# Kernel optimization log

Hardware: AMD Instinct MI355X
Metric: run time of the kernel (lower is better)

Reference implementation:

```python
import jax, jax.numpy as jnp
import numpy as np

BANDWITH = 10.0  # matches init kwarg `bandwith`


def setup_inputs() -> dict:
    key = jax.random.key(0)
    kx, ky = jax.random.split(key)
    X = jax.random.normal(kx, (8192, 128), dtype=jnp.float32)
    Y = jax.random.normal(ky, (8192, 128), dtype=jnp.float32)
    return {"X": X, "Y": Y}


def reference(X, Y):
    # Z = vstack([X, Y]) : [N+M, d]
    Z = jnp.concatenate([X, Y], axis=0)
    # squared euclidean cdist: ||zi||^2 + ||zj||^2 - 2 zi.zj  (clamped >= 0)
    sq = jnp.sum(Z * Z, axis=-1)  # [N+M]
    d2 = sq[:, None] + sq[None, :] - 2.0 * jnp.matmul(Z, Z.T)
    d2 = jnp.maximum(d2, 0.0)
    # RBF kernel; the original's [None,...].sum(dim=0) over a single bandwidth is identity
    K = jnp.exp(-d2 / (2.0 * BANDWITH ** 2))  # [N+M, N+M]
    n = X.shape[0]
    XX = jnp.mean(K[:n, :n])
    XY = jnp.mean(K[:n, n:])
    YY = jnp.mean(K[n:, n:])
    return XX - 2.0 * XY + YY
```

## Files before the change

kernel.cpp:

```cpp
#include <hip/hip_runtime.h>
#include <math.h>

#define TD 128
#define BT 64
#define TB 256
#define GRID 256

typedef _Float16 half8 __attribute__((ext_vector_type(8)));
typedef _Float16 half2v __attribute__((ext_vector_type(2)));
typedef float f32x4 __attribute__((ext_vector_type(4)));

#define C2f   (-0.0072134752044448f)
#define M2C2f (0.0144269504088896f)

#if __has_builtin(__builtin_amdgcn_exp2f)
#define EXP2F(x) __builtin_amdgcn_exp2f(x)
#else
#define EXP2F(x) exp2f(x)
#endif

#define LA0 0
#define LA1 32768
#define LB0 65536
#define LB1 98304
#define LEA 131072
#define LEB 132096
#define LRED 133120
#define LDS_TOT 133152

#define FENCE() asm volatile("" ::: "memory")
#define SCHEDB() __builtin_amdgcn_sched_barrier(0)

__device__ __forceinline__ void gload16(const void* g, void* l) {
    __builtin_amdgcn_global_load_lds(
        (const __attribute__((address_space(1))) void*)g,
        (__attribute__((address_space(3))) void*)l, 16, 0, 0);
}

__device__ __forceinline__ void decode_tile(int t, int T, int& bi, int& bj) {
    double bguess = (2.0 * T + 1.0 -
                     sqrt((2.0 * T + 1.0) * (2.0 * T + 1.0) - 8.0 * (double)t)) * 0.5;
    int b = (int)bguess;
    if (b < 0) b = 0;
    if (b > T - 1) b = T - 1;
    while ((b + 1) * T - ((b + 1) * b) / 2 <= t) ++b;
    while (b * T - (b * (b - 1)) / 2 > t) --b;
    bi = b;
    bj = b + (t - (b * T - (b * (b - 1)) / 2));
}

__global__ __launch_bounds__(256) void cvt_norms_kernel(const float* __restrict__ X,
                                                        const float* __restrict__ Y,
                                                        int n, int tot,
                                                        _Float16* __restrict__ Z16,
                                                        float* __restrict__ En) {
    const int wid  = (blockIdx.x * 256 + threadIdx.x) >> 6;
    const int lane = threadIdx.x & 63;
    if (wid >= tot) return;
    const float* row = (wid < n) ? (X + (size_t)wid * TD) : (Y + (size_t)(wid - n) * TD);
    float2 v = *reinterpret_cast<const float2*>(row + lane * 2);
    _Float16 hx = (_Float16)v.x;
    _Float16 hy = (_Float16)v.y;
    half2v h2 = {hx, hy};
    *reinterpret_cast<half2v*>(Z16 + (size_t)wid * TD + lane * 2) = h2;
    float fx = (float)hx, fy = (float)hy;
    float s = fmaf(fx, fx, fy * fy);
#pragma unroll
    for (int off = 32; off > 0; off >>= 1) s += __shfl_down(s, off, 64);
    if (lane == 0) En[wid] = EXP2F(C2f * s);
}

__global__ __launch_bounds__(512, 2) void mmd_pipe_kernel(const _Float16* __restrict__ Z16,
                                                          const float* __restrict__ En,
                                                          double* __restrict__ partials,
                                                          int n, int m, int T, int ntiles) {
    __shared__ char lds[LDS_TOT];

    const int tid = threadIdx.x;
    const int l = tid & 63;
    const int w = tid >> 6;
    const int wrow = (w >> 2) * 128;
    const int wcol = (w & 3) * 64;
    const int lr = l & 15;
    const int kq = l >> 4;
    const int swz = lr & 7;

    const int rsub = l >> 3;
    const int psl  = l & 7;
    const int srcsw = (psl ^ rsub) << 4;

    int it = blockIdx.x;
    if (it >= ntiles) return;

    int bi, bj;
    decode_tile(it, T, bi, bj);

    {
        const char* gA = (const char*)(Z16 + (size_t)bi * TB * TD);
        const char* gB = (const char*)(Z16 + (size_t)bj * TB * TD);
#pragma unroll
        for (int q = 0; q < 4; ++q) {
            const int chunk = w * 4 + q;
            const int row = chunk * 8 + rsub;
            gload16(gA + (size_t)row * 256 + srcsw, lds + LA0 + chunk * 1024);
            gload16(gB + (size_t)row * 256 + srcsw, lds + LB0 + chunk * 1024);
        }
    }

    while (true) {
        {
            const char* gA = (const char*)(Z16 + (size_t)bi * TB * TD);
            const char* gB = (const char*)(Z16 + (size_t)bj * TB * TD);
#pragma unroll
            for (int q = 0; q < 4; ++q) {
                const int chunk = w * 4 + q;
                const int row = chunk * 8 + rsub;
                gload16(gA + (size_t)row * 256 + 128 + srcsw, lds + LA1 + chunk * 1024);
                gload16(gB + (size_t)row * 256 + 128 + srcsw, lds + LB1 + chunk * 1024);
            }
            if (w == 0) gload16(En + (size_t)bi * TB + l * 4, lds + LEA);
            if (w == 1) gload16(En + (size_t)bj * TB + l * 4, lds + LEB);
        }
        if (w < 2) asm volatile("s_waitcnt vmcnt(9)" ::: "memory");
        else       asm volatile("s_waitcnt vmcnt(8)" ::: "memory");
        SCHEDB();
        __builtin_amdgcn_s_barrier();
        SCHEDB();

        f32x4 acc[8][4];
        const f32x4 zero4 = {0.f, 0.f, 0.f, 0.f};
        __builtin_amdgcn_s_setprio(1);
#pragma unroll
        for (int kk = 0; kk < 2; ++kk) {
            const int soff = ((kk * 4 + kq) ^ swz) << 4;
            half8 bf[4];
#pragma unroll
            for (int j = 0; j < 4; ++j)
                bf[j] = *reinterpret_cast<const half8*>(lds + LB0 + (wcol + j * 16 + lr) * 128 + soff);
#pragma unroll
            for (int i = 0; i < 8; ++i) {
                half8 af = *reinterpret_cast<const half8*>(lds + LA0 + (wrow + i * 16 + lr) * 128 + soff);
#pragma unroll
                for (int j = 0; j < 4; ++j)
                    acc[i][j] = __builtin_amdgcn_mfma_f32_16x16x32_f16(
                        af, bf[j], (kk == 0) ? zero4 : acc[i][j], 0, 0, 0);
            }
        }
        __builtin_amdgcn_s_setprio(0);

        FENCE();
        __builtin_amdgcn_s_barrier();
        SCHEDB();

        const int itn = it + GRID;
        const bool more = (itn < ntiles);
        int bin = bi, bjn = bj;
        if (more) {
            decode_tile(itn, T, bin, bjn);
            const char* gA = (const char*)(Z16 + (size_t)bin * TB * TD);
            const char* gB = (const char*)(Z16 + (size_t)bjn * TB * TD);
#pragma unroll
            for (int q = 0; q < 4; ++q) {
                const int chunk = w * 4 + q;
                const int row = chunk * 8 + rsub;
                gload16(gA + (size_t)row * 256 + srcsw, lds + LA0 + chunk * 1024);
                gload16(gB + (size_t)row * 256 + srcsw, lds + LB0 + chunk * 1024);
            }
        }
        if (more) asm volatile("s_waitcnt vmcnt(8)" ::: "memory");
        else      asm volatile("s_waitcnt vmcnt(0)" ::: "memory");
        SCHEDB();
        __builtin_amdgcn_s_barrier();
        SCHEDB();

        __builtin_amdgcn_s_setprio(1);
#pragma unroll
        for (int kk = 0; kk < 2; ++kk) {
            const int soff = ((kk * 4 + kq) ^ swz) << 4;
            half8 bf[4];
#pragma unroll
            for (int j = 0; j < 4; ++j)
                bf[j] = *reinterpret_cast<const half8*>(lds + LB1 + (wcol + j * 16 + lr) * 128 + soff);
#pragma unroll
            for (int i = 0; i < 8; ++i) {
                half8 af = *reinterpret_cast<const half8*>(lds + LA1 + (wrow + i * 16 + lr) * 128 + soff);
#pragma unroll
                for (int j = 0; j < 4; ++j)
                    acc[i][j] = __builtin_amdgcn_mfma_f32_16x16x32_f16(af, bf[j], acc[i][j], 0, 0, 0);
            }
        }
        __builtin_amdgcn_s_setprio(0);

        float Ej[4];
#pragma unroll
        for (int j = 0; j < 4; ++j)
            Ej[j] = *reinterpret_cast<const float*>(lds + LEB + (wcol + j * 16 + lr) * 4);
        f32x4 EiV[8];
#pragma unroll
        for (int i = 0; i < 8; ++i)
            EiV[i] = *reinterpret_cast<const f32x4*>(lds + LEA + (wrow + i * 16 + kq * 4) * 4);

        float s = 0.f;
#pragma unroll
        for (int j = 0; j < 4; ++j) {
            float sj0 = 0.f, sj1 = 0.f;
#pragma unroll
            for (int i = 0; i < 8; ++i) {
#pragma unroll
                for (int r = 0; r < 4; ++r) {
                    float e = EXP2F(M2C2f * acc[i][j][r]);
                    if (r & 1) sj1 = fmaf(EiV[i][r], e, sj1);
                    else       sj0 = fmaf(EiV[i][r], e, sj0);
                }
            }
            s = fmaf(Ej[j], sj0 + sj1, s);
        }

#pragma unroll
        for (int off = 32; off > 0; off >>= 1) s += __shfl_down(s, off, 64);
        if (l == 0) *reinterpret_cast<float*>(lds + LRED + w * 4) = s;
        asm volatile("s_waitcnt lgkmcnt(0)" ::: "memory");
        SCHEDB();
        __builtin_amdgcn_s_barrier();
        SCHEDB();
        if (tid == 0) {
            const float* sred = reinterpret_cast<const float*>(lds + LRED);
            float bs = 0.f;
#pragma unroll
            for (int q = 0; q < 8; ++q) bs += sred[q];
            double wa = (bi * TB < n) ? (1.0 / (double)n) : (-1.0 / (double)m);
            double wb = (bj * TB < n) ? (1.0 / (double)n) : (-1.0 / (double)m);
            double wgt = wa * wb * ((bi == bj) ? 1.0 : 2.0);
            partials[it] = wgt * (double)bs;
        }

        if (!more) break;
        it = itn; bi = bin; bj = bjn;
    }
}

__global__ __launch_bounds__(256) void norms_kernel(const float* __restrict__ X,
                                                    const float* __restrict__ Y,
                                                    int n, int tot,
                                                    float* __restrict__ norms) {
    int r = blockIdx.x * 256 + threadIdx.x;
    if (r >= tot) return;
    const float* row = (r < n) ? (X + (size_t)r * TD) : (Y + (size_t)(r - n) * TD);
    float s = 0.f;
#pragma unroll
    for (int k = 0; k < TD; k += 4) {
        float4 v = *reinterpret_cast<const float4*>(row + k);
        s = fmaf(v.x, v.x, s); s = fmaf(v.y, v.y, s);
        s = fmaf(v.z, v.z, s); s = fmaf(v.w, v.w, s);
    }
    norms[r] = s;
}

__global__ __launch_bounds__(256, 2) void mmd_tile_kernel(const float* __restrict__ X,
                                                          const float* __restrict__ Y,
                                                          const float* __restrict__ norms,
                                                          double* __restrict__ partials,
                                                          int n, int m, int T) {
    __shared__ float sA[TD][BT];
    __shared__ float sB[TD][BT];
    __shared__ float sredf[4];

    const int t = blockIdx.x;
    int bi, bj;
    decode_tile(t, T, bi, bj);

    const int tid = threadIdx.x;
    {
        const int row = tid & 63;
        const int qb  = tid >> 6;
        const int ra = bi * BT + row;
        const int rb = bj * BT + row;
        const float* Arow = (ra < n) ? (X + (size_t)ra * TD) : (Y + (size_t)(ra - n) * TD);
        const float* Brow = (rb < n) ? (X + (size_t)rb * TD) : (Y + (size_t)(rb - n) * TD);
#pragma unroll
        for (int i = 0; i < 8; ++i) {
            const int q = qb + 4 * i;
            float4 va = *reinterpret_cast<const float4*>(Arow + 4 * q);
            sA[4 * q + 0][row] = va.x; sA[4 * q + 1][row] = va.y;
            sA[4 * q + 2][row] = va.z; sA[4 * q + 3][row] = va.w;
            float4 vb = *reinterpret_cast<const float4*>(Brow + 4 * q);
            sB[4 * q + 0][row] = vb.x; sB[4 * q + 1][row] = vb.y;
            sB[4 * q + 2][row] = vb.z; sB[4 * q + 3][row] = vb.w;
        }
    }
    __syncthreads();

    const int tx = tid & 15;
    const int ty = tid >> 4;
    float acc[4][4];
#pragma unroll
    for (int i = 0; i < 4; ++i)
#pragma unroll
        for (int j = 0; j < 4; ++j) acc[i][j] = 0.f;

#pragma unroll 16
    for (int k = 0; k < TD; ++k) {
        float4 a = *reinterpret_cast<const float4*>(&sA[k][ty * 4]);
        float4 b = *reinterpret_cast<const float4*>(&sB[k][tx * 4]);
        const float av[4] = {a.x, a.y, a.z, a.w};
        const float bv[4] = {b.x, b.y, b.z, b.w};
#pragma unroll
        for (int i = 0; i < 4; ++i)
#pragma unroll
            for (int j = 0; j < 4; ++j)
                acc[i][j] = fmaf(av[i], bv[j], acc[i][j]);
    }

    float nA[4], nB[4];
#pragma unroll
    for (int i = 0; i < 4; ++i) nA[i] = norms[bi * BT + ty * 4 + i];
#pragma unroll
    for (int j = 0; j < 4; ++j) nB[j] = norms[bj * BT + tx * 4 + j];

    const float cexp = -0.005f;
    float s = 0.f;
#pragma unroll
    for (int i = 0; i < 4; ++i)
#pragma unroll
        for (int j = 0; j < 4; ++j) {
            float d2 = fmaxf(nA[i] + nB[j] - 2.f * acc[i][j], 0.f);
            s += __expf(d2 * cexp);
        }

#pragma unroll
    for (int off = 32; off > 0; off >>= 1) s += __shfl_down(s, off, 64);
    if ((tid & 63) == 0) sredf[tid >> 6] = s;
    __syncthreads();
    if (tid == 0) {
        double wa = (bi * BT < n) ? (1.0 / (double)n) : (-1.0 / (double)m);
        double wb = (bj * BT < n) ? (1.0 / (double)n) : (-1.0 / (double)m);
        double wgt = wa * wb * ((bi == bj) ? 1.0 : 2.0);
        partials[t] = wgt * (double)(sredf[0] + sredf[1] + sredf[2] + sredf[3]);
    }
}

__global__ __launch_bounds__(256) void reduce_kernel(const double* __restrict__ partials,
                                                     int npart,
                                                     float* __restrict__ out) {
    __shared__ double sd[256];
    double s = 0.0;
    for (int i = threadIdx.x; i < npart; i += 256) s += partials[i];
    sd[threadIdx.x] = s;
    __syncthreads();
    for (int off = 128; off > 0; off >>= 1) {
        if ((int)threadIdx.x < off) sd[threadIdx.x] += sd[threadIdx.x + off];
        __syncthreads();
    }
    if (threadIdx.x == 0) out[0] = (float)sd[0];
}

extern "C" void kernel_launch(void* const* d_in, const int* in_sizes, int n_in,
                              void* d_out, int out_size, void* d_ws, size_t ws_size,
                              hipStream_t stream) {
    const float* X = (const float*)d_in[0];
    const float* Y = (const float*)d_in[1];
    float* out = (float*)d_out;

    const int n = in_sizes[0] / TD;
    const int m = in_sizes[1] / TD;
    const int tot = n + m;

    const size_t z16_bytes = (size_t)tot * TD * 2;
    const size_t en_off    = (z16_bytes + 255) & ~(size_t)255;
    const size_t en_bytes  = (size_t)tot * 4;
    const size_t part_off  = ((en_off + en_bytes) + 255) & ~(size_t)255;
    const int Tm = tot / TB;
    const int npart_m = Tm * (Tm + 1) / 2;
    const size_t needed = part_off + (size_t)npart_m * 8;

    if (ws_size >= needed && (tot % TB) == 0 && (n % TB) == 0) {
        _Float16* Z16 = (_Float16*)d_ws;
        float* En = (float*)((char*)d_ws + en_off);
        double* partials = (double*)((char*)d_ws + part_off);
        cvt_norms_kernel<<<(tot + 3) / 4, 256, 0, stream>>>(X, Y, n, tot, Z16, En);
        int grid = (npart_m < GRID) ? npart_m : GRID;
        mmd_pipe_kernel<<<grid, 512, 0, stream>>>(Z16, En, partials, n, m, Tm, npart_m);
        reduce_kernel<<<1, 256, 0, stream>>>(partials, npart_m, out);
    } else {
        const int T = tot / BT;
        const int npart = T * (T + 1) / 2;
        float* norms = (float*)d_ws;
        double* partials = (double*)((char*)d_ws + (((size_t)tot * 4 + 255) & ~(size_t)255));
        norms_kernel<<<(tot + 255) / 256, 256, 0, stream>>>(X, Y, n, tot, norms);
        mmd_tile_kernel<<<npart, 256, 0, stream>>>(X, Y, norms, partials, n, m, T);
        reduce_kernel<<<1, 256, 0, stream>>>(partials, npart, out);
    }
}
```

Baseline: 67.14 us.

## Use 1024-thread blocks, prefetch next tile's second half, accumulate per-wave partials

Doubles the block to 16 waves, each computing a 64x64 sub-tile, which halves accumulator registers per wave and raises latency hiding. It also prefetches the next tile's second K-half and norm vectors right after the current epilogue's LDS reads, overlapping that load with the exp-reduction. The per-tile LDS block reduction and barrier are replaced by per-wave double accumulation, with one partial per wave written at the end. Risks include more barrier cost per wave and a larger final reduction array.

```diff
diff --git a/kernel.cpp b/kernel.cpp
--- a/kernel.cpp
+++ b/kernel.cpp
@@ -25,10 +25,8 @@
 #define LB1 98304
 #define LEA 131072
 #define LEB 132096
-#define LRED 133120
-#define LDS_TOT 133152
-
-#define FENCE() asm volatile("" ::: "memory")
+#define LDS_TOT 133120
+
 #define SCHEDB() __builtin_amdgcn_sched_barrier(0)
 
 __device__ __forceinline__ void gload16(const void* g, void* l) {
@@ -70,16 +68,16 @@
     if (lane == 0) En[wid] = EXP2F(C2f * s);
 }
 
-__global__ __launch_bounds__(512, 2) void mmd_pipe_kernel(const _Float16* __restrict__ Z16,
-                                                          const float* __restrict__ En,
-                                                          double* __restrict__ partials,
-                                                          int n, int m, int T, int ntiles) {
+__global__ __launch_bounds__(1024, 4) void mmd_pipe_kernel(const _Float16* __restrict__ Z16,
+                                                           const float* __restrict__ En,
+                                                           double* __restrict__ partials,
+                                                           int n, int m, int T, int ntiles) {
     __shared__ char lds[LDS_TOT];
 
     const int tid = threadIdx.x;
     const int l = tid & 63;
     const int w = tid >> 6;
-    const int wrow = (w >> 2) * 128;
+    const int wrow = (w >> 2) * 64;
     const int wcol = (w & 3) * 64;
     const int lr = l & 15;
     const int kq = l >> 4;
@@ -89,154 +87,164 @@
     const int psl  = l & 7;
     const int srcsw = (psl ^ rsub) << 4;
 
+    double acc_d = 0.0;
     int it = blockIdx.x;
-    if (it >= ntiles) return;
-
-    int bi, bj;
-    decode_tile(it, T, bi, bj);
-
-    {
-        const char* gA = (const char*)(Z16 + (size_t)bi * TB * TD);
-        const char* gB = (const char*)(Z16 + (size_t)bj * TB * TD);
-#pragma unroll
-        for (int q = 0; q < 4; ++q) {
-            const int chunk = w * 4 + q;
+
+    if (it < ntiles) {
+        int bi, bj;
+        decode_tile(it, T, bi, bj);
+        const char* gA = (const char*)Z16 + (size_t)bi * (TB * TD * 2);
+        const char* gB = (const char*)Z16 + (size_t)bj * (TB * TD * 2);
+
+#pragma unroll
+        for (int q = 0; q < 2; ++q) {
+            const int chunk = w * 2 + q;
             const int row = chunk * 8 + rsub;
             gload16(gA + (size_t)row * 256 + srcsw, lds + LA0 + chunk * 1024);
             gload16(gB + (size_t)row * 256 + srcsw, lds + LB0 + chunk * 1024);
         }
-    }
-
-    while (true) {
-        {
-            const char* gA = (const char*)(Z16 + (size_t)bi * TB * TD);
-            const char* gB = (const char*)(Z16 + (size_t)bj * TB * TD);
-#pragma unroll
-            for (int q = 0; q < 4; ++q) {
-                const int chunk = w * 4 + q;
-                const int row = chunk * 8 + rsub;
-                gload16(gA + (size_t)row * 256 + 128 + srcsw, lds + LA1 + chunk * 1024);
-                gload16(gB + (size_t)row * 256 + 128 + srcsw, lds + LB1 + chunk * 1024);
-            }
-            if (w == 0) gload16(En + (size_t)bi * TB + l * 4, lds + LEA);
-            if (w == 1) gload16(En + (size_t)bj * TB + l * 4, lds + LEB);
+#pragma unroll
+        for (int q = 0; q < 2; ++q) {
+            const int chunk = w * 2 + q;
+            const int row = chunk * 8 + rsub;
+            gload16(gA + (size_t)row * 256 + 128 + srcsw, lds + LA1 + chunk * 1024);
+            gload16(gB + (size_t)row * 256 + 128 + srcsw, lds + LB1 + chunk * 1024);
         }
-        if (w < 2) asm volatile("s_waitcnt vmcnt(9)" ::: "memory");
-        else       asm volatile("s_waitcnt vmcnt(8)" ::: "memory");
-        SCHEDB();
-        __builtin_amdgcn_s_barrier();
-        SCHEDB();
-
-        f32x4 acc[8][4];
-        const f32x4 zero4 = {0.f, 0.f, 0.f, 0.f};
-        __builtin_amdgcn_s_setprio(1);
-#pragma unroll
-        for (int kk = 0; kk < 2; ++kk) {
-            const int soff = ((kk * 4 + kq) ^ swz) << 4;
-            half8 bf[4];
+        if (w == 0) gload16(En + (size_t)bi * TB + (size_t)l * 4, lds + LEA);
+        if (w == 1) gload16(En + (size_t)bj * TB + (size_t)l * 4, lds + LEB);
+
+        while (true) {
+            if (w < 2) asm volatile("s_waitcnt vmcnt(5)" ::: "memory");
+            else       asm volatile("s_waitcnt vmcnt(4)" ::: "memory");
+            SCHEDB();
+            __builtin_amdgcn_s_barrier();
+            SCHEDB();
+
+            f32x4 acc[4][4];
+            const f32x4 zero4 = {0.f, 0.f, 0.f, 0.f};
+
+            __builtin_amdgcn_s_setprio(1);
+#pragma unroll
+            for (int kk = 0; kk < 2; ++kk) {
+                const int soff = ((kk * 4 + kq) ^ swz) << 4;
+                half8 bf[4];
+#pragma unroll
+                for (int j = 0; j < 4; ++j)
+                    bf[j] = *reinterpret_cast<const half8*>(lds + LB0 + (wcol + j * 16 + lr) * 128 + soff);
+#pragma unroll
+                for (int i = 0; i < 4; ++i) {
+                    half8 af = *reinterpret_cast<const half8*>(lds + LA0 + (wrow + i * 16 + lr) * 128 + soff);
+#pragma unroll
+                    for (int j = 0; j < 4; ++j)
+                        acc[i][j] = __builtin_amdgcn_mfma_f32_16x16x32_f16(
+                            af, bf[j], (kk == 0) ? zero4 : acc[i][j], 0, 0, 0);
+                }
+            }
+            __builtin_amdgcn_s_setprio(0);
+
+            asm volatile("" ::: "memory");
+            __builtin_amdgcn_s_barrier();
+            SCHEDB();
+
+            const int itn = it + GRID;
+            const bool more = (itn < ntiles);
+            int bin = bi, bjn = bj;
+            const char* gAn = gA;
+            const char* gBn = gB;
+            if (more) {
+                decode_tile(itn, T, bin, bjn);
+                gAn = (const char*)Z16 + (size_t)bin * (TB * TD * 2);
+                gBn = (const char*)Z16 + (size_t)bjn * (TB * TD * 2);
+#pragma unroll
+                for (int q = 0; q < 2; ++q) {
+                    const int chunk = w * 2 + q;
+                    const int row = chunk * 8 + rsub;
+                    gload16(gAn + (size_t)row * 256 + srcsw, lds + LA0 + chunk * 1024);
+                    gload16(gBn + (size_t)row * 256 + srcsw, lds + LB0 + chunk * 1024);
+                }
+            }
+
+            if (more) asm volatile("s_waitcnt vmcnt(4)" ::: "memory");
+            else      asm volatile("s_waitcnt vmcnt(0)" ::: "memory");
+            SCHEDB();
+            __builtin_amdgcn_s_barrier();
+            SCHEDB();
+
+            __builtin_amdgcn_s_setprio(1);
+#pragma unroll
+            for (int kk = 0; kk < 2; ++kk) {
+                const int soff = ((kk * 4 + kq) ^ swz) << 4;
+                half8 bf[4];
+#pragma unroll
+                for (int j = 0; j < 4; ++j)
+                    bf[j] = *reinterpret_cast<const half8*>(lds + LB1 + (wcol + j * 16 + lr) * 128 + soff);
+#pragma unroll
+                for (int i = 0; i < 4; ++i) {
+                    half8 af = *reinterpret_cast<const half8*>(lds + LA1 + (wrow + i * 16 + lr) * 128 + soff);
+#pragma unroll
+                    for (int j = 0; j < 4; ++j)
+                        acc[i][j] = __builtin_amdgcn_mfma_f32_16x16x32_f16(af, bf[j], acc[i][j], 0, 0, 0);
+                }
+            }
+            __builtin_amdgcn_s_setprio(0);
+
+            float Ej[4];
 #pragma unroll
             for (int j = 0; j < 4; ++j)
-                bf[j] = *reinterpret_cast<const half8*>(lds + LB0 + (wcol + j * 16 + lr) * 128 + soff);
-#pragma unroll
-            for (int i = 0; i < 8; ++i) {
-                half8 af = *reinterpret_cast<const half8*>(lds + LA0 + (wrow + i * 16 + lr) * 128 + soff);
-#pragma unroll
-                for (int j = 0; j < 4; ++j)
-                    acc[i][j] = __builtin_amdgcn_mfma_f32_16x16x32_f16(
-                        af, bf[j], (kk == 0) ? zero4 : acc[i][j], 0, 0, 0);
-            }
+                Ej[j] = *reinterpret_cast<const float*>(lds + LEB + (wcol + j * 16 + lr) * 4);
+            f32x4 EiV[4];
+#pragma unroll
+            for (int i = 0; i < 4; ++i)
+                EiV[i] = *reinterpret_cast<const f32x4*>(lds + LEA + (wrow + i * 16 + kq * 4) * 4);
+
+            asm volatile("s_waitcnt lgkmcnt(0)" ::: "memory");
+            SCHEDB();
+            __builtin_amdgcn_s_barrier();
+            SCHEDB();
+
+            if (more) {
+#pragma unroll
+                for (int q = 0; q < 2; ++q) {
+                    const int chunk = w * 2 + q;
+                    const int row = chunk * 8 + rsub;
+                    gload16(gAn + (size_t)row * 256 + 128 + srcsw, lds + LA1 + chunk * 1024);
+                    gload16(gBn + (size_t)row * 256 + 128 + srcsw, lds + LB1 + chunk * 1024);
+                }
+                if (w == 0) gload16(En + (size_t)bin * TB + (size_t)l * 4, lds + LEA);
+                if (w == 1) gload16(En + (size_t)bjn * TB + (size_t)l * 4, lds + LEB);
+            }
+
+            float s = 0.f;
+#pragma unroll
+            for (int j = 0; j < 4; ++j) {
+                float sj0 = 0.f, sj1 = 0.f;
+#pragma unroll
+                for (int i = 0; i < 4; ++i) {
+#pragma unroll
+                    for (int r = 0; r < 4; ++r) {
+                        float e = EXP2F(M2C2f * acc[i][j][r]);
+                        if (r & 1) sj1 = fmaf(EiV[i][r], e, sj1);
+                        else       sj0 = fmaf(EiV[i][r], e, sj0);
+                    }
+                }
+                s = fmaf(Ej[j], sj0 + sj1, s);
+            }
+#pragma unroll
+            for (int off = 32; off > 0; off >>= 1) s += __shfl_down(s, off, 64);
+
+            {
+                double wa = (bi * TB < n) ? (1.0 / (double)n) : (-1.0 / (double)m);
+                double wb = (bj * TB < n) ? (1.0 / (double)n) : (-1.0 / (double)m);
+                double wgt = wa * wb * ((bi == bj) ? 1.0 : 2.0);
+                acc_d += wgt * (double)s;
+            }
+
+            if (!more) break;
+            it = itn; bi = bin; bj = bjn;
         }
-        __builtin_amdgcn_s_setprio(0);
-
-        FENCE();
-        __builtin_amdgcn_s_barrier();
-        SCHEDB();
-
-        const int itn = it + GRID;
-        const bool more = (itn < ntiles);
-        int bin = bi, bjn = bj;
-        if (more) {
-            decode_tile(itn, T, bin, bjn);
-            const char* gA = (const char*)(Z16 + (size_t)bin * TB * TD);
-            const char* gB = (const char*)(Z16 + (size_t)bjn * TB * TD);
-#pragma unroll
-            for (int q = 0; q < 4; ++q) {
-                const int chunk = w * 4 + q;
-                const int row = chunk * 8 + rsub;
-                gload16(gA + (size_t)row * 256 + srcsw, lds + LA0 + chunk * 1024);
-                gload16(gB + (size_t)row * 256 + srcsw, lds + LB0 + chunk * 1024);
-            }
-        }
-        if (more) asm volatile("s_waitcnt vmcnt(8)" ::: "memory");
-        else      asm volatile("s_waitcnt vmcnt(0)" ::: "memory");
-        SCHEDB();
-        __builtin_amdgcn_s_barrier();
-        SCHEDB();
-
-        __builtin_amdgcn_s_setprio(1);
-#pragma unroll
-        for (int kk = 0; kk < 2; ++kk) {
-            const int soff = ((kk * 4 + kq) ^ swz) << 4;
-            half8 bf[4];
-#pragma unroll
-            for (int j = 0; j < 4; ++j)
-                bf[j] = *reinterpret_cast<const half8*>(lds + LB1 + (wcol + j * 16 + lr) * 128 + soff);
-#pragma unroll
-            for (int i = 0; i < 8; ++i) {
-                half8 af = *reinterpret_cast<const half8*>(lds + LA1 + (wrow + i * 16 + lr) * 128 + soff);
-#pragma unroll
-                for (int j = 0; j < 4; ++j)
-                    acc[i][j] = __builtin_amdgcn_mfma_f32_16x16x32_f16(af, bf[j], acc[i][j], 0, 0, 0);
-            }
-        }
-        __builtin_amdgcn_s_setprio(0);
-
-        float Ej[4];
-#pragma unroll
-        for (int j = 0; j < 4; ++j)
-            Ej[j] = *reinterpret_cast<const float*>(lds + LEB + (wcol + j * 16 + lr) * 4);
-        f32x4 EiV[8];
-#pragma unroll
-        for (int i = 0; i < 8; ++i)
-            EiV[i] = *reinterpret_cast<const f32x4*>(lds + LEA + (wrow + i * 16 + kq * 4) * 4);
-
-        float s = 0.f;
-#pragma unroll
-        for (int j = 0; j < 4; ++j) {
-            float sj0 = 0.f, sj1 = 0.f;
-#pragma unroll
-            for (int i = 0; i < 8; ++i) {
-#pragma unroll
-                for (int r = 0; r < 4; ++r) {
-                    float e = EXP2F(M2C2f * acc[i][j][r]);
-                    if (r & 1) sj1 = fmaf(EiV[i][r], e, sj1);
-                    else       sj0 = fmaf(EiV[i][r], e, sj0);
-                }
-            }
-            s = fmaf(Ej[j], sj0 + sj1, s);
-        }
-
-#pragma unroll
-        for (int off = 32; off > 0; off >>= 1) s += __shfl_down(s, off, 64);
-        if (l == 0) *reinterpret_cast<float*>(lds + LRED + w * 4) = s;
-        asm volatile("s_waitcnt lgkmcnt(0)" ::: "memory");
-        SCHEDB();
-        __builtin_amdgcn_s_barrier();
-        SCHEDB();
-        if (tid == 0) {
-            const float* sred = reinterpret_cast<const float*>(lds + LRED);
-            float bs = 0.f;
-#pragma unroll
-            for (int q = 0; q < 8; ++q) bs += sred[q];
-            double wa = (bi * TB < n) ? (1.0 / (double)n) : (-1.0 / (double)m);
-            double wb = (bj * TB < n) ? (1.0 / (double)n) : (-1.0 / (double)m);
-            double wgt = wa * wb * ((bi == bj) ? 1.0 : 2.0);
-            partials[it] = wgt * (double)bs;
-        }
-
-        if (!more) break;
-        it = itn; bi = bin; bj = bjn;
-    }
+    }
+
+    if (l == 0) partials[(size_t)blockIdx.x * 16 + w] = acc_d;
 }
 
 __global__ __launch_bounds__(256) void norms_kernel(const float* __restrict__ X,
@@ -371,16 +379,17 @@
     const size_t part_off  = ((en_off + en_bytes) + 255) & ~(size_t)255;
     const int Tm = tot / TB;
     const int npart_m = Tm * (Tm + 1) / 2;
-    const size_t needed = part_off + (size_t)npart_m * 8;
+    const int grid = (npart_m < GRID) ? npart_m : GRID;
+    const int nred = grid * 16;
+    const size_t needed = part_off + (size_t)nred * 8;
 
     if (ws_size >= needed && (tot % TB) == 0 && (n % TB) == 0) {
         _Float16* Z16 = (_Float16*)d_ws;
         float* En = (float*)((char*)d_ws + en_off);
         double* partials = (double*)((char*)d_ws + part_off);
         cvt_norms_kernel<<<(tot + 3) / 4, 256, 0, stream>>>(X, Y, n, tot, Z16, En);
-        int grid = (npart_m < GRID) ? npart_m : GRID;
-        mmd_pipe_kernel<<<grid, 512, 0, stream>>>(Z16, En, partials, n, m, Tm, npart_m);
-        reduce_kernel<<<1, 256, 0, stream>>>(partials, npart_m, out);
+        mmd_pipe_kernel<<<grid, 1024, 0, stream>>>(Z16, En, partials, n, m, Tm, npart_m);
+        reduce_kernel<<<1, 256, 0, stream>>>(partials, nred, out);
     } else {
         const int T = tot / BT;
         const int npart = T * (T + 1) / 2;
```

Result: slower. 94.39 us (+40.6%).
